# Kernel optimization log

Measured on AMD Instinct MI355X. Metric: run time of the kernel, lower is better.

Reference implementation:

```python
import jax, jax.numpy as jnp
import numpy as np

D_MODEL = 128; N_HEADS = 8; N_LEVELS = 1; N_POINTS = 8
MAX_RES = 10.0
B, H_SP, W_SP = 8, 64, 64


def setup_inputs() -> dict:
    key = jax.random.key(0)
    ks = jax.random.split(key, 8)
    s = 0.02
    f32 = jnp.float32
    return {
        "nbr_fea": jax.random.normal(ks[0], (B, D_MODEL, H_SP, W_SP), f32),
        "ext_fea": jax.random.normal(ks[1], (B, D_MODEL, H_SP, W_SP), f32),
        "W_val": jax.random.normal(ks[2], (D_MODEL, D_MODEL), f32) * s,
        "b_val": jnp.zeros((D_MODEL,), f32),
        "W_off": jax.random.normal(ks[3], (D_MODEL, N_HEADS * N_LEVELS * N_POINTS * 2), f32) * s,
        "b_off": jax.random.normal(ks[4], (N_HEADS * N_LEVELS * N_POINTS * 2,), f32) * s,
        "W_attn": jax.random.normal(ks[5], (D_MODEL, N_HEADS * N_LEVELS * N_POINTS), f32) * s,
        "b_attn": jnp.zeros((N_HEADS * N_LEVELS * N_POINTS,), f32),
        "W_out": jax.random.normal(ks[6], (D_MODEL, D_MODEL), f32) * s,
        "b_out": jnp.zeros((D_MODEL,), f32),
    }


def _deform_attn_align(nbr_fea, ext_fea, W_val, b_val, W_off, b_off, W_attn, b_attn, W_out, b_out):
    b, c, h, w = nbr_fea.shape
    L = h * w
    dh = c // N_HEADS
    # flatten b c h w -> b (h w) c
    query = jnp.transpose(ext_fea, (0, 2, 3, 1)).reshape(b, L, c)
    vin = jnp.transpose(nbr_fea, (0, 2, 3, 1)).reshape(b, L, c)

    # value projection (mask is all-False -> no masked fill needed)
    value = (vin @ W_val + b_val).reshape(b, L, N_HEADS, dh)
    vh = jnp.transpose(value, (0, 2, 1, 3))  # [b, H, L, dh]

    # sampling offsets, clamped by max_residue_magnitude * tanh
    off = MAX_RES * jnp.tanh(query @ W_off + b_off)
    off = off.reshape(b, L, N_HEADS, N_POINTS, 2)  # single level
    attn = jax.nn.softmax((query @ W_attn + b_attn).reshape(b, L, N_HEADS, N_POINTS), axis=-1)

    # reference points in [0,1]; valid_ratio == 1 since padding mask is all-False
    yy, xx = jnp.meshgrid(jnp.arange(h, dtype=jnp.float32), jnp.arange(w, dtype=jnp.float32), indexing="ij")
    ref = jnp.stack([(xx.reshape(-1) + 0.5) / w, (yy.reshape(-1) + 0.5) / h], axis=-1)  # [L, 2]
    norm = jnp.array([w, h], jnp.float32)  # offset_normalizer [W, H]
    loc = ref[None, :, None, None, :] + off / norm  # [b, L, H, P, 2]

    # grid_sample(align_corners=False, padding_mode='zeros') pixel coordinates
    px = jnp.transpose(loc[..., 0] * w - 0.5, (0, 2, 1, 3))  # [b, H, L, P]
    py = jnp.transpose(loc[..., 1] * h - 0.5, (0, 2, 1, 3))

    x0 = jnp.floor(px); y0 = jnp.floor(py)
    fx = px - x0; fy = py - y0
    x0i = x0.astype(jnp.int32); y0i = y0.astype(jnp.int32)

    def gather(xi, yi):
        valid = (xi >= 0) & (xi < w) & (yi >= 0) & (yi < h)
        idx = jnp.clip(yi, 0, h - 1) * w + jnp.clip(xi, 0, w - 1)  # [b, H, L, P]
        g = jnp.take_along_axis(vh, idx.reshape(b, N_HEADS, L * N_POINTS)[..., None], axis=2)
        return g.reshape(b, N_HEADS, L, N_POINTS, dh) * valid[..., None]

    samp = (gather(x0i, y0i) * ((1.0 - fx) * (1.0 - fy))[..., None]
            + gather(x0i + 1, y0i) * (fx * (1.0 - fy))[..., None]
            + gather(x0i, y0i + 1) * ((1.0 - fx) * fy)[..., None]
            + gather(x0i + 1, y0i + 1) * (fx * fy)[..., None])  # [b, H, L, P, dh]

    aw = jnp.transpose(attn, (0, 2, 1, 3))  # [b, H, L, P]
    out = jnp.sum(samp * aw[..., None], axis=3)  # [b, H, L, dh]
    out = jnp.transpose(out, (0, 2, 1, 3)).reshape(b, L, c)
    out = out @ W_out + b_out
    return jnp.transpose(out.reshape(b, h, w, c), (0, 3, 1, 2))  # b c h w


def reference(nbr_fea, ext_fea, W_val, b_val, W_off, b_off, W_attn, b_attn, W_out, b_out):
    return _deform_attn_align(nbr_fea, ext_fea, W_val, b_val, W_off, b_off, W_attn, b_attn, W_out, b_out)
```

## Files before the change

### kernel.cpp

```cpp
#include <hip/hip_runtime.h>
#include <cstdint>

#define HB 8
#define CM 128
#define NHEAD 8
#define NPT 8
#define DHD 16
#define HS 64
#define WS 64
#define LTOT 4096
#define NQA 192
#define QAP 192
#define LFP 132

typedef float floatx4 __attribute__((ext_vector_type(4)));
typedef short bf16x8 __attribute__((ext_vector_type(8)));

__device__ __forceinline__ unsigned short f2bf_rne(float x) {
  unsigned u = __float_as_uint(x);
  return (unsigned short)((u + 0x7FFFu + ((u >> 16) & 1)) >> 16);
}
__device__ __forceinline__ void split_bf(float x, unsigned short& h, unsigned short& l) {
  unsigned u = __float_as_uint(x);
  h = (unsigned short)(u >> 16);
  float r = x - __uint_as_float(u & 0xFFFF0000u);
  l = (unsigned short)(__float_as_uint(r) >> 16);
}
__device__ __forceinline__ float fast_tanh(float x) {
  float e = __expf(2.0f * x);
  return 1.0f - 2.0f / (e + 1.0f);
}

__global__ __launch_bounds__(256) void prep(const float* __restrict__ Wv,
                                            const float* __restrict__ Wo,
                                            const float* __restrict__ Wa,
                                            const float* __restrict__ Ww,
                                            const float* __restrict__ bo,
                                            const float* __restrict__ ba,
                                            unsigned short* __restrict__ wf_val,
                                            unsigned short* __restrict__ wf_qa,
                                            unsigned short* __restrict__ wf_out,
                                            float* __restrict__ bias_qa) {
  const int gid = blockIdx.x * 256 + threadIdx.x;
  const int k4 = gid / 448;
  const int ng = gid - k4 * 448;

  const float* src;
  unsigned short* dst;
  int Nsrc, Nn, nd, n;
  if (ng < 128) {        src = Wv; dst = wf_val; Nsrc = 128; Nn = 128; n = ng;        nd = n; }
  else if (ng < 256) {   src = Wo; dst = wf_qa;  Nsrc = 128; Nn = 192; n = ng - 128;  nd = n; }
  else if (ng < 320) {   src = Wa; dst = wf_qa;  Nsrc = 64;  Nn = 192; n = ng - 256;  nd = n + 128; }
  else {                 src = Ww; dst = wf_out; Nsrc = 128; Nn = 128; n = ng - 320;  nd = n; }

  ushort4 hi, lo;
  split_bf(src[(k4 * 4 + 0) * Nsrc + n], hi.x, lo.x);
  split_bf(src[(k4 * 4 + 1) * Nsrc + n], hi.y, lo.y);
  split_bf(src[(k4 * 4 + 2) * Nsrc + n], hi.z, lo.z);
  split_bf(src[(k4 * 4 + 3) * Nsrc + n], hi.w, lo.w);
  const int off = (k4 >> 1) * Nn * 8 + nd * 8 + (k4 & 1) * 4;
  *(ushort4*)(dst + off) = hi;
  *(ushort4*)(dst + Nn * 128 + off) = lo;

  if (gid < 128) bias_qa[gid] = bo[gid];
  else if (gid < 192) bias_qa[gid] = ba[gid - 128];
}

__global__ __launch_bounds__(256, 4) void gemm_val(const float* __restrict__ nbr,
                                                   const unsigned short* __restrict__ WF,
                                                   const float* __restrict__ bias,
                                                   unsigned short* __restrict__ value) {
  __shared__ char smem[33792];
  unsigned short* AB = (unsigned short*)smem;
  const int t = threadIdx.x;
  const int ml0 = blockIdx.x * 64;
  const int b = blockIdx.y;

  {
    const float* src = nbr + (size_t)b * CM * LTOT + ml0;
    const int x = t & 63, kq = t >> 6;
#pragma unroll
    for (int i = 0; i < 8; i++) {
      const int kb = kq * 4 + i * 16;
      ushort4 hi, lo;
      split_bf(src[(size_t)(kb + 0) * LTOT + x], hi.x, lo.x);
      split_bf(src[(size_t)(kb + 1) * LTOT + x], hi.y, lo.y);
      split_bf(src[(size_t)(kb + 2) * LTOT + x], hi.z, lo.z);
      split_bf(src[(size_t)(kb + 3) * LTOT + x], hi.w, lo.w);
      const int off = x * 128 + (((kb >> 3) ^ (x & 15)) << 3) + (kb & 7);
      *(ushort4*)(AB + off) = hi;
      *(ushort4*)(AB + 8192 + off) = lo;
    }
  }
  __syncthreads();

  const int w = t >> 6, lane = t & 63;
  const int wm = (w >> 1) * 32, wn = (w & 1) * 64;
  const int nl = lane & 15, q = lane >> 4;

  floatx4 acc[2][4];
#pragma unroll
  for (int mt = 0; mt < 2; mt++)
#pragma unroll
    for (int j = 0; j < 4; j++) acc[mt][j] = {0.0f, 0.0f, 0.0f, 0.0f};

#pragma unroll
  for (int K0 = 0; K0 < 4; K0++) {
    bf16x8 ah[2], al[2];
#pragma unroll
    for (int mt = 0; mt < 2; mt++) {
      const int m = wm + mt * 16 + nl;
      const int off = m * 128 + (((K0 * 4 + q) ^ (m & 15)) << 3);
      ah[mt] = *(bf16x8*)(AB + off);
      al[mt] = *(bf16x8*)(AB + 8192 + off);
    }
#pragma unroll
    for (int j = 0; j < 4; j++) {
      const size_t o = (size_t)(K0 * 4 + q) * CM * 8 + (wn + j * 16 + nl) * 8;
      const bf16x8 wh = *(const bf16x8*)(WF + o);
      const bf16x8 wl = *(const bf16x8*)(WF + (size_t)CM * 128 + o);
#pragma unroll
      for (int mt = 0; mt < 2; mt++) {
        acc[mt][j] = __builtin_amdgcn_mfma_f32_16x16x32_bf16(al[mt], wh, acc[mt][j], 0, 0, 0);
        acc[mt][j] = __builtin_amdgcn_mfma_f32_16x16x32_bf16(ah[mt], wl, acc[mt][j], 0, 0, 0);
        acc[mt][j] = __builtin_amdgcn_mfma_f32_16x16x32_bf16(ah[mt], wh, acc[mt][j], 0, 0, 0);
      }
    }
  }

  __syncthreads();
  float* LF = (float*)smem;
#pragma unroll
  for (int j = 0; j < 4; j++) {
    const int gc = wn + j * 16 + nl;
    const float bv = bias[gc];
#pragma unroll
    for (int mt = 0; mt < 2; mt++)
#pragma unroll
      for (int r = 0; r < 4; r++)
        LF[(wm + mt * 16 + q * 4 + r) * LFP + gc] = acc[mt][j][r] + bv;
  }
  __syncthreads();
#pragma unroll
  for (int i = 0; i < 4; i++) {
    const int c = t + i * 256;
    const int h = c >> 7, rem = c & 127, l = rem >> 1, half = rem & 1;
    const float* sp = LF + l * LFP + h * 16 + half * 8;
    uint4 st;
    st.x = ((unsigned)f2bf_rne(sp[1]) << 16) | f2bf_rne(sp[0]);
    st.y = ((unsigned)f2bf_rne(sp[3]) << 16) | f2bf_rne(sp[2]);
    st.z = ((unsigned)f2bf_rne(sp[5]) << 16) | f2bf_rne(sp[4]);
    st.w = ((unsigned)f2bf_rne(sp[7]) << 16) | f2bf_rne(sp[6]);
    *(uint4*)(value + ((size_t)(b * NHEAD + h) * LTOT + ml0 + l) * DHD + half * 8) = st;
  }
}

__global__ __launch_bounds__(256, 4) void samp(const float* __restrict__ ext,
                                               const unsigned short* __restrict__ value,
                                               const unsigned short* __restrict__ wf_qa,
                                               const unsigned short* __restrict__ wf_out,
                                               const float* __restrict__ bias_qa,
                                               const float* __restrict__ b_out,
                                               float* __restrict__ out) {
  __shared__ char smem[40960];
  unsigned short* AB = (unsigned short*)smem;
  float* qaT = (float*)(smem + 16384);
  float2* WXY = (float2*)smem;
  float* WA = (float*)(smem + 16384);
  unsigned short* FR = (unsigned short*)(smem + 24576);

  const int t = threadIdx.x;
  const int b = blockIdx.x & 7;
  const int ml0 = (blockIdx.x >> 3) * 32;
  const int w = t >> 6, lane = t & 63;
  const int nl = lane & 15, q = lane >> 4;

  {
    const float* src = ext + (size_t)b * CM * LTOT + ml0;
    const int x = t & 31, kq = t >> 5;
#pragma unroll
    for (int i = 0; i < 4; i++) {
      const int kb = i * 32 + kq * 4;
      ushort4 hi, lo;
      split_bf(src[(size_t)(kb + 0) * LTOT + x], hi.x, lo.x);
      split_bf(src[(size_t)(kb + 1) * LTOT + x], hi.y, lo.y);
      split_bf(src[(size_t)(kb + 2) * LTOT + x], hi.z, lo.z);
      split_bf(src[(size_t)(kb + 3) * LTOT + x], hi.w, lo.w);
      const int off = x * 128 + (((kb >> 3) ^ (x & 15)) << 3) + (kb & 7);
      *(ushort4*)(AB + off) = hi;
      *(ushort4*)(AB + 4096 + off) = lo;
    }
  }
  __syncthreads();

  {
    const int wm = (w & 1) * 16;
    const int wn = (w >> 1) * 96;
    floatx4 acc[6];
#pragma unroll
    for (int j = 0; j < 6; j++) acc[j] = {0.0f, 0.0f, 0.0f, 0.0f};
#pragma unroll
    for (int K0 = 0; K0 < 4; K0++) {
      const int m = wm + nl;
      const int off = m * 128 + (((K0 * 4 + q) ^ (m & 15)) << 3);
      const bf16x8 ah = *(bf16x8*)(AB + off);
      const bf16x8 al = *(bf16x8*)(AB + 4096 + off);
#pragma unroll
      for (int j = 0; j < 6; j++) {
        const size_t o = (size_t)(K0 * 4 + q) * NQA * 8 + (wn + j * 16 + nl) * 8;
        const bf16x8 wh = *(const bf16x8*)(wf_qa + o);
        const bf16x8 wl = *(const bf16x8*)(wf_qa + (size_t)NQA * 128 + o);
        acc[j] = __builtin_amdgcn_mfma_f32_16x16x32_bf16(al, wh, acc[j], 0, 0, 0);
        acc[j] = __builtin_amdgcn_mfma_f32_16x16x32_bf16(ah, wl, acc[j], 0, 0, 0);
        acc[j] = __builtin_amdgcn_mfma_f32_16x16x32_bf16(ah, wh, acc[j], 0, 0, 0);
      }
    }
#pragma unroll
    for (int j = 0; j < 6; j++) {
      const int n = wn + j * 16 + nl;
      const float bv = bias_qa[n];
#pragma unroll
      for (int r = 0; r < 4; r++)
        qaT[(wm + q * 4 + r) * QAP + n] = acc[j][r] + bv;
    }
  }
  __syncthreads();

  {
    const int ll = t >> 3, h = t & 7;
    const float* qrow = qaT + ll * QAP;
    float4 of[4];
#pragma unroll
    for (int j = 0; j < 4; j++) of[j] = *(const float4*)(qrow + h * 16 + j * 4);
    const float4 lga = *(const float4*)(qrow + 128 + h * 8);
    const float4 lgb = *(const float4*)(qrow + 128 + h * 8 + 4);
    __syncthreads();
    const float lg[8] = {lga.x, lga.y, lga.z, lga.w, lgb.x, lgb.y, lgb.z, lgb.w};
    float m = lg[0];
#pragma unroll
    for (int p = 1; p < 8; p++) m = fmaxf(m, lg[p]);
    float e[8], s = 0.0f;
#pragma unroll
    for (int p = 0; p < 8; p++) { e[p] = __expf(lg[p] - m); s += e[p]; }
    const float inv = 1.0f / s;
    const int l = ml0 + ll;
    const float xf = (float)(l & (WS - 1));
    const float yf = (float)(l >> 6);
#pragma unroll
    for (int p = 0; p < 8; p++) {
      const float ox = (p & 1) ? of[p >> 1].z : of[p >> 1].x;
      const float oy = (p & 1) ? of[p >> 1].w : of[p >> 1].y;
      WXY[p * 256 + t] = {xf + 10.0f * fast_tanh(ox), yf + 10.0f * fast_tanh(oy)};
      WA[p * 256 + t] = e[p] * inv;
    }
  }
  __syncthreads();

  {
    const int d4 = t & 3;
    const int u = t >> 2;
#pragma unroll
    for (int ps = 0; ps < 4; ps++) {
      const int uu = ps * 64 + u;
      const int ll = uu >> 3;
      const int h = uu & 7;
      const unsigned short* vbb = value + ((size_t)(b * NHEAD + h) * LTOT) * DHD + d4 * 4;

      float4 o = {0.0f, 0.0f, 0.0f, 0.0f};
#pragma unroll
      for (int p = 0; p < 8; p++) {
        const float2 pxy = WXY[p * 256 + uu];
        const float aw = WA[p * 256 + uu];
        const float x0f = floorf(pxy.x), y0f = floorf(pxy.y);
        const float fx = pxy.x - x0f, fy = pxy.y - y0f;
        const int ix = (int)x0f, iy = (int)y0f;
#pragma unroll
        for (int c = 0; c < 4; c++) {
          const int cdx = c & 1, cdy = c >> 1;
          const int jx = ix + cdx, jy = iy + cdy;
          const float wx = cdx ? fx : 1.0f - fx;
          const float wy = cdy ? fy : 1.0f - fy;
          const bool valid = ((unsigned)jx < WS) & ((unsigned)jy < HS);
          const float wc = valid ? aw * wx * wy : 0.0f;
          const int cx = min(max(jx, 0), WS - 1);
          const int cy = min(max(jy, 0), HS - 1);
          const uint2 rw = *(const uint2*)(vbb + (size_t)((cy << 6) + cx) * DHD);
          o.x += wc * __uint_as_float(rw.x << 16);
          o.y += wc * __uint_as_float(rw.x & 0xFFFF0000u);
          o.z += wc * __uint_as_float(rw.y << 16);
          o.w += wc * __uint_as_float(rw.y & 0xFFFF0000u);
        }
      }
      const int off = ll * 128 + (((h * 2 + (d4 >> 1)) ^ (ll & 15)) << 3) + (d4 & 1) * 4;
      ushort4 st = {f2bf_rne(o.x), f2bf_rne(o.y), f2bf_rne(o.z), f2bf_rne(o.w)};
      *(ushort4*)(FR + off) = st;
    }
  }
  __syncthreads();

  {
    const int wm = (w & 1) * 16;
    const int wn = (w >> 1) * 64;
    floatx4 acc[4];
#pragma unroll
    for (int j = 0; j < 4; j++) acc[j] = {0.0f, 0.0f, 0.0f, 0.0f};
#pragma unroll
    for (int K0 = 0; K0 < 4; K0++) {
      const int m = wm + nl;
      const int off = m * 128 + (((K0 * 4 + q) ^ (m & 15)) << 3);
      const bf16x8 ah = *(bf16x8*)(FR + off);
#pragma unroll
      for (int j = 0; j < 4; j++) {
        const int n = wn + j * 16 + nl;
        const size_t o = (size_t)(K0 * 4 + q) * CM * 8 + n * 8;
        const bf16x8 wh = *(const bf16x8*)(wf_out + o);
        const bf16x8 wl = *(const bf16x8*)(wf_out + (size_t)CM * 128 + o);
        acc[j] = __builtin_amdgcn_mfma_f32_16x16x32_bf16(ah, wl, acc[j], 0, 0, 0);
        acc[j] = __builtin_amdgcn_mfma_f32_16x16x32_bf16(ah, wh, acc[j], 0, 0, 0);
      }
    }
#pragma unroll
    for (int j = 0; j < 4; j++) {
      const int gc = wn + j * 16 + nl;
      const float bv = b_out[gc];
      float4 st = {acc[j][0] + bv, acc[j][1] + bv, acc[j][2] + bv, acc[j][3] + bv};
      *(float4*)(out + ((size_t)b * CM + gc) * LTOT + ml0 + wm + q * 4) = st;
    }
  }
}

extern "C" void kernel_launch(void* const* d_in, const int* in_sizes, int n_in,
                              void* d_out, int out_size, void* d_ws, size_t ws_size,
                              hipStream_t stream) {
  const float* nbr    = (const float*)d_in[0];
  const float* ext    = (const float*)d_in[1];
  const float* W_val  = (const float*)d_in[2];
  const float* b_val  = (const float*)d_in[3];
  const float* W_off  = (const float*)d_in[4];
  const float* b_off  = (const float*)d_in[5];
  const float* W_attn = (const float*)d_in[6];
  const float* b_attn = (const float*)d_in[7];
  const float* W_out  = (const float*)d_in[8];
  const float* b_out  = (const float*)d_in[9];
  float* out = (float*)d_out;

  unsigned short* value = (unsigned short*)d_ws;
  unsigned short* wf_val = value + (size_t)HB * NHEAD * LTOT * DHD;
  unsigned short* wf_qa  = wf_val + 128 * 128 * 2;
  unsigned short* wf_out = wf_qa + 192 * 128 * 2;
  float* bias_qa = (float*)(wf_out + 128 * 128 * 2);

  prep<<<56, 256, 0, stream>>>(W_val, W_off, W_attn, W_out, b_off, b_attn,
                               wf_val, wf_qa, wf_out, bias_qa);
  gemm_val<<<dim3(64, HB), 256, 0, stream>>>(nbr, wf_val, b_val, value);
  samp<<<dim3(128 * HB), 256, 0, stream>>>(ext, value, wf_qa, wf_out, bias_qa, b_out, out);
}
```

Before: 135.5 us.

## Keep sampling locations in registers, gather full 16-channel rows per thread

The sampling stage no longer writes per-point locations and attention weights to shared memory. Each thread keeps its own query/head's 8 points in registers and gathers whole 32-byte value rows (two uint4 loads per corner), instead of four threads each fetching 8 bytes. Shared memory shrinks from 40 KB to about 25 KB by aliasing buffers, the qaT row pitch is padded to 196 to reduce bank conflicts, and launch bounds rise to 5 blocks per CU. The cost is higher register pressure per thread and less parallelism per gather, which could cause spills or leave memory latency less hidden.

```diff
diff --git a/kernel.cpp b/kernel.cpp
--- a/kernel.cpp
+++ b/kernel.cpp
@@ -10,7 +10,7 @@
 #define WS 64
 #define LTOT 4096
 #define NQA 192
-#define QAP 192
+#define QAP 196
 #define LFP 132
 
 typedef float floatx4 __attribute__((ext_vector_type(4)));
@@ -29,6 +29,14 @@
 __device__ __forceinline__ float fast_tanh(float x) {
   float e = __expf(2.0f * x);
   return 1.0f - 2.0f / (e + 1.0f);
+}
+__device__ __forceinline__ void bf8_fma(floatx4& oa, floatx4& ob, const uint4 r, const float wc) {
+  floatx4 va = {__uint_as_float(r.x << 16), __uint_as_float(r.x & 0xFFFF0000u),
+                __uint_as_float(r.y << 16), __uint_as_float(r.y & 0xFFFF0000u)};
+  floatx4 vb = {__uint_as_float(r.z << 16), __uint_as_float(r.z & 0xFFFF0000u),
+                __uint_as_float(r.w << 16), __uint_as_float(r.w & 0xFFFF0000u)};
+  oa += va * wc;
+  ob += vb * wc;
 }
 
 __global__ __launch_bounds__(256) void prep(const float* __restrict__ Wv,
@@ -70,7 +78,7 @@
                                                    const unsigned short* __restrict__ WF,
                                                    const float* __restrict__ bias,
                                                    unsigned short* __restrict__ value) {
-  __shared__ char smem[33792];
+  __shared__ __align__(16) char smem[33792];
   unsigned short* AB = (unsigned short*)smem;
   const int t = threadIdx.x;
   const int ml0 = blockIdx.x * 64;
@@ -155,19 +163,17 @@
   }
 }
 
-__global__ __launch_bounds__(256, 4) void samp(const float* __restrict__ ext,
+__global__ __launch_bounds__(256, 5) void samp(const float* __restrict__ ext,
                                                const unsigned short* __restrict__ value,
                                                const unsigned short* __restrict__ wf_qa,
                                                const unsigned short* __restrict__ wf_out,
                                                const float* __restrict__ bias_qa,
                                                const float* __restrict__ b_out,
                                                float* __restrict__ out) {
-  __shared__ char smem[40960];
+  __shared__ __align__(16) char smem[25088];
   unsigned short* AB = (unsigned short*)smem;
-  float* qaT = (float*)(smem + 16384);
-  float2* WXY = (float2*)smem;
-  float* WA = (float*)(smem + 16384);
-  unsigned short* FR = (unsigned short*)(smem + 24576);
+  float* qaT = (float*)smem;
+  unsigned short* FR = (unsigned short*)smem;
 
   const int t = threadIdx.x;
   const int b = blockIdx.x & 7;
@@ -215,6 +221,7 @@
         acc[j] = __builtin_amdgcn_mfma_f32_16x16x32_bf16(ah, wh, acc[j], 0, 0, 0);
       }
     }
+    __syncthreads();
 #pragma unroll
     for (int j = 0; j < 6; j++) {
       const int n = wn + j * 16 + nl;
@@ -226,15 +233,15 @@
   }
   __syncthreads();
 
-  {
-    const int ll = t >> 3, h = t & 7;
+  float px[8], py[8], aw[8];
+  const int ll = t >> 3, h = t & 7;
+  {
     const float* qrow = qaT + ll * QAP;
     float4 of[4];
 #pragma unroll
     for (int j = 0; j < 4; j++) of[j] = *(const float4*)(qrow + h * 16 + j * 4);
     const float4 lga = *(const float4*)(qrow + 128 + h * 8);
     const float4 lgb = *(const float4*)(qrow + 128 + h * 8 + 4);
-    __syncthreads();
     const float lg[8] = {lga.x, lga.y, lga.z, lga.w, lgb.x, lgb.y, lgb.z, lgb.w};
     float m = lg[0];
 #pragma unroll
@@ -250,50 +257,66 @@
     for (int p = 0; p < 8; p++) {
       const float ox = (p & 1) ? of[p >> 1].z : of[p >> 1].x;
       const float oy = (p & 1) ? of[p >> 1].w : of[p >> 1].y;
-      WXY[p * 256 + t] = {xf + 10.0f * fast_tanh(ox), yf + 10.0f * fast_tanh(oy)};
-      WA[p * 256 + t] = e[p] * inv;
-    }
-  }
-  __syncthreads();
-
-  {
-    const int d4 = t & 3;
-    const int u = t >> 2;
-#pragma unroll
-    for (int ps = 0; ps < 4; ps++) {
-      const int uu = ps * 64 + u;
-      const int ll = uu >> 3;
-      const int h = uu & 7;
-      const unsigned short* vbb = value + ((size_t)(b * NHEAD + h) * LTOT) * DHD + d4 * 4;
-
-      float4 o = {0.0f, 0.0f, 0.0f, 0.0f};
-#pragma unroll
-      for (int p = 0; p < 8; p++) {
-        const float2 pxy = WXY[p * 256 + uu];
-        const float aw = WA[p * 256 + uu];
-        const float x0f = floorf(pxy.x), y0f = floorf(pxy.y);
-        const float fx = pxy.x - x0f, fy = pxy.y - y0f;
-        const int ix = (int)x0f, iy = (int)y0f;
-#pragma unroll
-        for (int c = 0; c < 4; c++) {
-          const int cdx = c & 1, cdy = c >> 1;
-          const int jx = ix + cdx, jy = iy + cdy;
-          const float wx = cdx ? fx : 1.0f - fx;
-          const float wy = cdy ? fy : 1.0f - fy;
-          const bool valid = ((unsigned)jx < WS) & ((unsigned)jy < HS);
-          const float wc = valid ? aw * wx * wy : 0.0f;
-          const int cx = min(max(jx, 0), WS - 1);
-          const int cy = min(max(jy, 0), HS - 1);
-          const uint2 rw = *(const uint2*)(vbb + (size_t)((cy << 6) + cx) * DHD);
-          o.x += wc * __uint_as_float(rw.x << 16);
-          o.y += wc * __uint_as_float(rw.x & 0xFFFF0000u);
-          o.z += wc * __uint_as_float(rw.y << 16);
-          o.w += wc * __uint_as_float(rw.y & 0xFFFF0000u);
-        }
-      }
-      const int off = ll * 128 + (((h * 2 + (d4 >> 1)) ^ (ll & 15)) << 3) + (d4 & 1) * 4;
-      ushort4 st = {f2bf_rne(o.x), f2bf_rne(o.y), f2bf_rne(o.z), f2bf_rne(o.w)};
-      *(ushort4*)(FR + off) = st;
+      px[p] = xf + 10.0f * fast_tanh(ox);
+      py[p] = yf + 10.0f * fast_tanh(oy);
+      aw[p] = e[p] * inv;
+    }
+  }
+  __syncthreads();
+
+  {
+    const unsigned hb = (unsigned)(b * NHEAD + h) * LTOT * DHD;
+    floatx4 o0 = {0.f, 0.f, 0.f, 0.f}, o1 = o0, o2 = o0, o3 = o0;
+#pragma unroll
+    for (int p = 0; p < 8; p++) {
+      const float x0f = floorf(px[p]), y0f = floorf(py[p]);
+      const float fx = px[p] - x0f, fy = py[p] - y0f;
+      const int ix = (int)x0f, iy = (int)y0f;
+      const float a = aw[p];
+      float wc[4];
+      unsigned adr[4];
+#pragma unroll
+      for (int c = 0; c < 4; c++) {
+        const int cdx = c & 1, cdy = c >> 1;
+        const int jx = ix + cdx, jy = iy + cdy;
+        const float wx = cdx ? fx : 1.0f - fx;
+        const float wy = cdy ? fy : 1.0f - fy;
+        const bool valid = ((unsigned)jx < WS) & ((unsigned)jy < HS);
+        wc[c] = valid ? a * wx * wy : 0.0f;
+        const int cx = min(max(jx, 0), WS - 1);
+        const int cy = min(max(jy, 0), HS - 1);
+        adr[c] = hb + (unsigned)((cy << 6) + cx) * DHD;
+      }
+      uint4 r0[4], r1[4];
+#pragma unroll
+      for (int c = 0; c < 4; c++) {
+        r0[c] = *(const uint4*)(value + adr[c]);
+        r1[c] = *(const uint4*)(value + adr[c] + 8);
+      }
+#pragma unroll
+      for (int c = 0; c < 4; c++) {
+        bf8_fma(o0, o1, r0[c], wc[c]);
+        bf8_fma(o2, o3, r1[c], wc[c]);
+      }
+    }
+    const int llm = ll & 15;
+    {
+      const int off = ll * 128 + (((h * 2 + 0) ^ llm) << 3);
+      uint4 st;
+      st.x = ((unsigned)f2bf_rne(o0[1]) << 16) | f2bf_rne(o0[0]);
+      st.y = ((unsigned)f2bf_rne(o0[3]) << 16) | f2bf_rne(o0[2]);
+      st.z = ((unsigned)f2bf_rne(o1[1]) << 16) | f2bf_rne(o1[0]);
+      st.w = ((unsigned)f2bf_rne(o1[3]) << 16) | f2bf_rne(o1[2]);
+      *(uint4*)(FR + off) = st;
+    }
+    {
+      const int off = ll * 128 + (((h * 2 + 1) ^ llm) << 3);
+      uint4 st;
+      st.x = ((unsigned)f2bf_rne(o2[1]) << 16) | f2bf_rne(o2[0]);
+      st.y = ((unsigned)f2bf_rne(o2[3]) << 16) | f2bf_rne(o2[2]);
+      st.z = ((unsigned)f2bf_rne(o3[1]) << 16) | f2bf_rne(o3[0]);
+      st.w = ((unsigned)f2bf_rne(o3[3]) << 16) | f2bf_rne(o3[2]);
+      *(uint4*)(FR + off) = st;
     }
   }
   __syncthreads();
```

New measurement: 276.9 us. +104.3%, slower.
